# Kernel optimization log

Measured on AMD Instinct MI355X. Metric: run time of the kernel, lower is better.

The kernel has to match this reference:

```python
import jax, jax.numpy as jnp
import numpy as np

B, N, E, M = 16, 128, 127, 16
BN = B * N
BNE = B * N * E


def _ln(x, g, b):
    mu = x.mean(-1, keepdims=True)
    var = ((x - mu) ** 2).mean(-1, keepdims=True)
    return (x - mu) * jax.lax.rsqrt(var + 1e-5) * g + b


def _radial(feat, w1, b1, g1, be1, w2, b2, g2, be2, w3, b3, nf):
    # Linear -> LayerNorm -> ReLU -> Linear -> LayerNorm -> ReLU -> Linear
    h = jax.nn.relu(_ln(feat @ w1.T + b1, g1, be1))
    h = jax.nn.relu(_ln(h @ w2.T + b2, g2, be2))
    y = h @ w3.T + b3
    return y.reshape(-1, M, 1, M, 1, nf)  # [BN, out_ch, 1, in_ch, 1, num_freq]


def _kernel(R, basis, do):
    K = (R * basis).sum(-1)  # [BN, M, 2do+1, M, 2di+1]
    return K.reshape(K.shape[0], (2 * do + 1) * M, -1)


def setup_inputs() -> dict:
    key = jax.random.key(0)
    ks = jax.random.split(key, 16)
    d = {}
    d["r"] = jax.random.uniform(ks[0], (BNE, 1), jnp.float32)
    d["src0"] = jax.random.normal(ks[1], (BNE, M, 1), jnp.float32)
    d["src1"] = jax.random.normal(ks[2], (BNE, M, 3), jnp.float32)
    d["basis_00"] = jax.random.normal(ks[3], (BN, 1, 1, 1, 1, 1), jnp.float32)
    d["basis_01"] = jax.random.normal(ks[4], (BN, 1, 3, 1, 1, 1), jnp.float32)
    d["basis_10"] = jax.random.normal(ks[5], (BN, 1, 1, 1, 3, 1), jnp.float32)
    d["basis_11"] = jax.random.normal(ks[6], (BN, 1, 3, 1, 3, 3), jnp.float32)
    d["w1"] = jax.random.normal(ks[7], (4, 32, 1), jnp.float32) * 0.5
    d["b1"] = jnp.zeros((4, 32), jnp.float32)
    d["g1"] = jnp.ones((4, 32), jnp.float32)
    d["be1"] = jnp.zeros((4, 32), jnp.float32)
    d["w2"] = jax.random.normal(ks[8], (4, 32, 32), jnp.float32) * 0.18
    d["b2"] = jnp.zeros((4, 32), jnp.float32)
    d["g2"] = jnp.ones((4, 32), jnp.float32)
    d["be2"] = jnp.zeros((4, 32), jnp.float32)
    d["w3_00"] = jax.random.normal(ks[9], (1 * M * M, 32), jnp.float32) * 0.18
    d["b3_00"] = jnp.zeros((1 * M * M,), jnp.float32)
    d["w3_01"] = jax.random.normal(ks[10], (1 * M * M, 32), jnp.float32) * 0.18
    d["b3_01"] = jnp.zeros((1 * M * M,), jnp.float32)
    d["w3_10"] = jax.random.normal(ks[11], (1 * M * M, 32), jnp.float32) * 0.18
    d["b3_10"] = jnp.zeros((1 * M * M,), jnp.float32)
    d["w3_11"] = jax.random.normal(ks[12], (3 * M * M, 32), jnp.float32) * 0.18
    d["b3_11"] = jnp.zeros((3 * M * M,), jnp.float32)
    return d


def reference(r, src0, src1, basis_00, basis_01, basis_10, basis_11,
              w1, b1, g1, be1, w2, b2, g2, be2,
              w3_00, b3_00, w3_01, b3_01, w3_10, b3_10, w3_11, b3_11):
    # reduce per-edge tensors to the representative (first) edge of each node,
    # exactly as the original's view(B,N,E,...)[:, :, 0] does
    feat = r.reshape(B, N, E, -1)[:, :, 0, :].reshape(BN, -1)             # [BN, 1]
    s0 = src0.reshape(B, N, E, M * 1, 1)[:, :, 0].reshape(BN, M * 1, 1)   # [BN, 16, 1]
    s1 = src1.reshape(B, N, E, M * 3, 1)[:, :, 0].reshape(BN, M * 48 // M, 1)  # [BN, 48, 1]

    # per-(d_in, d_out) kernels; param index 0=(0,0) 1=(0,1) 2=(1,0) 3=(1,1)
    K00 = _kernel(_radial(feat, w1[0], b1[0], g1[0], be1[0], w2[0], b2[0], g2[0], be2[0], w3_00, b3_00, 1), basis_00, 0)
    K01 = _kernel(_radial(feat, w1[1], b1[1], g1[1], be1[1], w2[1], b2[1], g2[1], be2[1], w3_01, b3_01, 1), basis_01, 1)
    K10 = _kernel(_radial(feat, w1[2], b1[2], g1[2], be1[2], w2[2], b2[2], g2[2], be2[2], w3_10, b3_10, 1), basis_10, 0)
    K11 = _kernel(_radial(feat, w1[3], b1[3], g1[3], be1[3], w2[3], b2[3], g2[3], be2[3], w3_11, b3_11, 3), basis_11, 1)

    msg0 = K00 @ s0 + K10 @ s1  # [BN, 16, 1]  (degree-0 output)
    msg1 = K01 @ s0 + K11 @ s1  # [BN, 48, 1]  (degree-1 output)

    # broadcast per-node message to every edge of that node
    out0 = jnp.broadcast_to(msg0.reshape(B, N, 1, M, 1), (B, N, E, M, 1)).reshape(BNE, M, 1)
    out1 = jnp.broadcast_to(msg1.reshape(B, N, 1, M * 3, 1), (B, N, E, M * 3, 1)).reshape(BNE, M, 3)
    return out0, out1
```

## Files before the change

### kernel.cpp

```cpp
#include <hip/hip_runtime.h>

#define E_ 127
#define NB 8
#define OUT0_F4 1040384
#define O0_PER_NODE_F4 508
#define O1_PER_NODE_F4 1524

__device__ __forceinline__ float red32(float v) {
    v += __shfl_xor(v, 1, 32);
    v += __shfl_xor(v, 2, 32);
    v += __shfl_xor(v, 4, 32);
    v += __shfl_xor(v, 8, 32);
    v += __shfl_xor(v, 16, 32);
    return v;
}

__global__ __launch_bounds__(256) void msg_kernel(
    const float* __restrict__ r,   const float* __restrict__ src0, const float* __restrict__ src1,
    const float* __restrict__ b00, const float* __restrict__ b01,
    const float* __restrict__ b10, const float* __restrict__ b11,
    const float* __restrict__ w1,  const float* __restrict__ bb1,
    const float* __restrict__ g1,  const float* __restrict__ be1,
    const float* __restrict__ w2,  const float* __restrict__ bb2,
    const float* __restrict__ g2,  const float* __restrict__ be2,
    const float* __restrict__ w300, const float* __restrict__ b300,
    const float* __restrict__ w301, const float* __restrict__ b301,
    const float* __restrict__ w310, const float* __restrict__ b310,
    const float* __restrict__ w311, const float* __restrict__ b311,
    float* __restrict__ msg_out)
{
    __shared__ float s0s[NB][16];
    __shared__ float s1s[NB][48];
    __shared__ float t1s[NB][16];
    __shared__ float us[NB][3][16][3];
    __shared__ float b00s[NB];
    __shared__ float b01s[NB][3];
    __shared__ float b10s[NB][3];
    __shared__ float b11s[NB][27];
    __shared__ float feats[NB];
    __shared__ float h2s[4][NB][32];
    __shared__ float Rl[NB][1537];

    const int tid = threadIdx.x;
    const int n0 = blockIdx.x * NB;

    for (int idx = tid; idx < NB * 16; idx += 256) {
        int nn = idx >> 4, m = idx & 15;
        s0s[nn][m] = src0[(size_t)(n0 + nn) * E_ * 16 + m];
    }
    for (int idx = tid; idx < NB * 48; idx += 256) {
        int nn = idx / 48, j = idx % 48;
        s1s[nn][j] = src1[(size_t)(n0 + nn) * E_ * 48 + j];
    }
    if (tid < NB) {
        b00s[tid]  = b00[n0 + tid];
        feats[tid] = r[(size_t)(n0 + tid) * E_];
    }
    if (tid >= 32 && tid < 32 + NB * 3) {
        int q = tid - 32; int nn = q / 3, d = q % 3;
        b01s[nn][d] = b01[(size_t)(n0 + nn) * 3 + d];
    }
    if (tid >= 64 && tid < 64 + NB * 3) {
        int q = tid - 64; int nn = q / 3, c = q % 3;
        b10s[nn][c] = b10[(size_t)(n0 + nn) * 3 + c];
    }
    for (int idx = tid; idx < NB * 27; idx += 256) {
        int nn = idx / 27, q = idx % 27;
        b11s[nn][q] = b11[(size_t)(n0 + nn) * 27 + q];
    }
    __syncthreads();

    for (int idx = tid; idx < NB * 16; idx += 256) {
        int nn = idx >> 4, i = idx & 15;
        t1s[nn][i] = b10s[nn][0] * s1s[nn][i*3]
                   + b10s[nn][1] * s1s[nn][i*3+1]
                   + b10s[nn][2] * s1s[nn][i*3+2];
    }
    for (int idx = tid; idx < NB * 144; idx += 256) {
        int nn = idx / 144, q = idx % 144;
        int d = q / 48, q2 = q % 48, i = q2 / 3, f = q2 % 3;
        float a = 0.f;
        #pragma unroll
        for (int c = 0; c < 3; ++c) a += b11s[nn][d*9 + c*3 + f] * s1s[nn][i*3 + c];
        us[nn][d][i][f] = a;
    }

    {
        const int g = tid >> 5;
        const int j = tid & 31;
        #pragma unroll
        for (int p = 0; p < 4; ++p) {
            float h = feats[g] * w1[p*32 + j] + bb1[p*32 + j];
            float mu = red32(h) * (1.0f/32.0f);
            float dv = h - mu;
            float var = red32(dv*dv) * (1.0f/32.0f);
            float x = dv * rsqrtf(var + 1e-5f) * g1[p*32 + j] + be1[p*32 + j];
            float h1n = fmaxf(x, 0.0f);

            const float4* w2v = (const float4*)(w2 + p*1024 + j*32);
            float acc = bb2[p*32 + j];
            #pragma unroll
            for (int k4 = 0; k4 < 8; ++k4) {
                float4 w = w2v[k4];
                acc += __shfl(h1n, 4*k4 + 0, 32) * w.x;
                acc += __shfl(h1n, 4*k4 + 1, 32) * w.y;
                acc += __shfl(h1n, 4*k4 + 2, 32) * w.z;
                acc += __shfl(h1n, 4*k4 + 3, 32) * w.w;
            }
            mu = red32(acc) * (1.0f/32.0f);
            dv = acc - mu;
            var = red32(dv*dv) * (1.0f/32.0f);
            x = dv * rsqrtf(var + 1e-5f) * g2[p*32 + j] + be2[p*32 + j];
            h2s[p][g][j] = fmaxf(x, 0.0f);
        }
    }
    __syncthreads();

    for (int rr = 0; rr < 6; ++rr) {
        int idx = tid + rr * 256;
        const float* W; const float* Bv; int p, row;
        if (idx < 256)      { p = 0; row = idx;       W = w300; Bv = b300; }
        else if (idx < 512) { p = 1; row = idx - 256; W = w301; Bv = b301; }
        else if (idx < 768) { p = 2; row = idx - 512; W = w310; Bv = b310; }
        else                { p = 3; row = idx - 768; W = w311; Bv = b311; }
        const float4* wv = (const float4*)(W + row * 32);
        float4 a0 = wv[0], a1 = wv[1], a2 = wv[2], a3 = wv[3];
        float4 a4 = wv[4], a5 = wv[5], a6 = wv[6], a7 = wv[7];
        float bb = Bv[row];
        #pragma unroll
        for (int nn = 0; nn < NB; ++nn) {
            const float* h = h2s[p][nn];
            float acc = bb;
            acc += a0.x*h[0]  + a0.y*h[1]  + a0.z*h[2]  + a0.w*h[3];
            acc += a1.x*h[4]  + a1.y*h[5]  + a1.z*h[6]  + a1.w*h[7];
            acc += a2.x*h[8]  + a2.y*h[9]  + a2.z*h[10] + a2.w*h[11];
            acc += a3.x*h[12] + a3.y*h[13] + a3.z*h[14] + a3.w*h[15];
            acc += a4.x*h[16] + a4.y*h[17] + a4.z*h[18] + a4.w*h[19];
            acc += a5.x*h[20] + a5.y*h[21] + a5.z*h[22] + a5.w*h[23];
            acc += a6.x*h[24] + a6.y*h[25] + a6.z*h[26] + a6.w*h[27];
            acc += a7.x*h[28] + a7.y*h[29] + a7.z*h[30] + a7.w*h[31];
            Rl[nn][idx] = acc;
        }
    }
    __syncthreads();

    for (int pair = tid; pair < 512; pair += 256) {
        if (pair < 128) {
            int o = pair >> 3, nn = pair & 7;
            const float* Rn = Rl[nn];
            float acc0 = 0.f, acc2 = 0.f;
            #pragma unroll
            for (int i = 0; i < 16; ++i) {
                acc0 += Rn[o*16 + i]       * s0s[nn][i];
                acc2 += Rn[512 + o*16 + i] * t1s[nn][i];
            }
            msg_out[(size_t)(n0 + nn) * 64 + o] = b00s[nn] * acc0 + acc2;
        } else {
            int q = pair - 128;
            int od = q >> 3, nn = q & 7;
            int o = od / 3, d = od % 3;
            const float* Rn = Rl[nn];
            float acc1 = 0.f, acc3 = 0.f;
            #pragma unroll
            for (int i = 0; i < 16; ++i) {
                acc1 += Rn[256 + o*16 + i] * s0s[nn][i];
                #pragma unroll
                for (int f = 0; f < 3; ++f)
                    acc3 += Rn[768 + (o*16 + i)*3 + f] * us[nn][d][i][f];
            }
            msg_out[(size_t)(n0 + nn) * 64 + 16 + od] = b01s[nn][d] * acc1 + acc3;
        }
    }
}

__global__ __launch_bounds__(256) void bcast_kernel(const float* __restrict__ msg,
                                                    float* __restrict__ out)
{
    __shared__ float4 m0v[4];
    __shared__ float4 m1v[12];
    const int n = blockIdx.x;
    const int tid = threadIdx.x;
    if (tid < 16) {
        float4 v = ((const float4*)(msg + (size_t)n * 64))[tid];
        if (tid < 4) m0v[tid] = v; else m1v[tid - 4] = v;
    }
    __syncthreads();

    float4* o0 = (float4*)out + (size_t)n * O0_PER_NODE_F4;
    for (int k = tid; k < O0_PER_NODE_F4; k += 256)
        o0[k] = m0v[k & 3];

    float4* o1 = (float4*)out + OUT0_F4 + (size_t)n * O1_PER_NODE_F4;
    for (int k = tid; k < O1_PER_NODE_F4; k += 256)
        o1[k] = m1v[k % 12];
}

extern "C" void kernel_launch(void* const* d_in, const int* in_sizes, int n_in,
                              void* d_out, int out_size, void* d_ws, size_t ws_size,
                              hipStream_t stream)
{
    const float* r    = (const float*)d_in[0];
    const float* src0 = (const float*)d_in[1];
    const float* src1 = (const float*)d_in[2];
    const float* b00  = (const float*)d_in[3];
    const float* b01  = (const float*)d_in[4];
    const float* b10  = (const float*)d_in[5];
    const float* b11  = (const float*)d_in[6];
    const float* w1   = (const float*)d_in[7];
    const float* bb1  = (const float*)d_in[8];
    const float* g1   = (const float*)d_in[9];
    const float* be1  = (const float*)d_in[10];
    const float* w2   = (const float*)d_in[11];
    const float* bb2  = (const float*)d_in[12];
    const float* g2   = (const float*)d_in[13];
    const float* be2  = (const float*)d_in[14];
    const float* w300 = (const float*)d_in[15];
    const float* b300 = (const float*)d_in[16];
    const float* w301 = (const float*)d_in[17];
    const float* b301 = (const float*)d_in[18];
    const float* w310 = (const float*)d_in[19];
    const float* b310 = (const float*)d_in[20];
    const float* w311 = (const float*)d_in[21];
    const float* b311 = (const float*)d_in[22];

    float* msg = (float*)d_ws;

    msg_kernel<<<256, 256, 0, stream>>>(r, src0, src1, b00, b01, b10, b11,
        w1, bb1, g1, be1, w2, bb2, g2, be2,
        w300, b300, w301, b301, w310, b310, w311, b311, msg);

    bcast_kernel<<<2048, 256, 0, stream>>>(msg, (float*)d_out);
}
```

Measured before the change: 172.5 us.

## Fuse message computation and edge broadcast into one kernel with smaller node batches

Merges the per-node message kernel and the broadcast kernel into a single kernel, so messages stay in shared memory and go straight to the output without a workspace round trip or a second launch. The node batch per block is halved so the grid doubles to 512 blocks. Thread-to-work mappings for loads, the radial MLP and the contraction are remapped to fit 4 nodes per block. In exchange, the bandwidth-bound broadcast now runs on only 512 blocks that must first finish the MLP compute, which may reduce store parallelism.

```diff
diff --git a/kernel.cpp b/kernel.cpp
--- a/kernel.cpp
+++ b/kernel.cpp
@@ -1,7 +1,7 @@
 #include <hip/hip_runtime.h>
 
 #define E_ 127
-#define NB 8
+#define NB 4
 #define OUT0_F4 1040384
 #define O0_PER_NODE_F4 508
 #define O1_PER_NODE_F4 1524
@@ -15,7 +15,7 @@
     return v;
 }
 
-__global__ __launch_bounds__(256) void msg_kernel(
+__global__ __launch_bounds__(256) void fused_kernel(
     const float* __restrict__ r,   const float* __restrict__ src0, const float* __restrict__ src1,
     const float* __restrict__ b00, const float* __restrict__ b01,
     const float* __restrict__ b10, const float* __restrict__ b11,
@@ -27,7 +27,7 @@
     const float* __restrict__ w301, const float* __restrict__ b301,
     const float* __restrict__ w310, const float* __restrict__ b310,
     const float* __restrict__ w311, const float* __restrict__ b311,
-    float* __restrict__ msg_out)
+    float* __restrict__ out)
 {
     __shared__ float s0s[NB][16];
     __shared__ float s1s[NB][48];
@@ -40,45 +40,46 @@
     __shared__ float feats[NB];
     __shared__ float h2s[4][NB][32];
     __shared__ float Rl[NB][1537];
+    __shared__ float msgs[NB][64];
 
     const int tid = threadIdx.x;
     const int n0 = blockIdx.x * NB;
 
-    for (int idx = tid; idx < NB * 16; idx += 256) {
-        int nn = idx >> 4, m = idx & 15;
+    if (tid < NB * 16) {
+        int nn = tid >> 4, m = tid & 15;
         s0s[nn][m] = src0[(size_t)(n0 + nn) * E_ * 16 + m];
     }
-    for (int idx = tid; idx < NB * 48; idx += 256) {
-        int nn = idx / 48, j = idx % 48;
+    if (tid >= 64 && tid < 64 + NB * 48) {
+        int q = tid - 64; int nn = q / 48, j = q % 48;
         s1s[nn][j] = src1[(size_t)(n0 + nn) * E_ * 48 + j];
     }
     if (tid < NB) {
         b00s[tid]  = b00[n0 + tid];
         feats[tid] = r[(size_t)(n0 + tid) * E_];
     }
-    if (tid >= 32 && tid < 32 + NB * 3) {
-        int q = tid - 32; int nn = q / 3, d = q % 3;
+    if (tid >= 8 && tid < 8 + NB * 3) {
+        int q = tid - 8; int nn = q / 3, d = q % 3;
         b01s[nn][d] = b01[(size_t)(n0 + nn) * 3 + d];
     }
-    if (tid >= 64 && tid < 64 + NB * 3) {
-        int q = tid - 64; int nn = q / 3, c = q % 3;
+    if (tid >= 24 && tid < 24 + NB * 3) {
+        int q = tid - 24; int nn = q / 3, c = q % 3;
         b10s[nn][c] = b10[(size_t)(n0 + nn) * 3 + c];
     }
-    for (int idx = tid; idx < NB * 27; idx += 256) {
-        int nn = idx / 27, q = idx % 27;
-        b11s[nn][q] = b11[(size_t)(n0 + nn) * 27 + q];
-    }
-    __syncthreads();
-
-    for (int idx = tid; idx < NB * 16; idx += 256) {
-        int nn = idx >> 4, i = idx & 15;
+    if (tid >= 40 && tid < 40 + NB * 27) {
+        int q = tid - 40; int nn = q / 27, qq = q % 27;
+        b11s[nn][qq] = b11[(size_t)(n0 + nn) * 27 + qq];
+    }
+    __syncthreads();
+
+    if (tid < NB * 16) {
+        int nn = tid >> 4, i = tid & 15;
         t1s[nn][i] = b10s[nn][0] * s1s[nn][i*3]
                    + b10s[nn][1] * s1s[nn][i*3+1]
                    + b10s[nn][2] * s1s[nn][i*3+2];
     }
     for (int idx = tid; idx < NB * 144; idx += 256) {
-        int nn = idx / 144, q = idx % 144;
-        int d = q / 48, q2 = q % 48, i = q2 / 3, f = q2 % 3;
+        int nn = idx / 144, qq = idx % 144;
+        int d = qq / 48, q2 = qq % 48, i = q2 / 3, f = q2 % 3;
         float a = 0.f;
         #pragma unroll
         for (int c = 0; c < 3; ++c) a += b11s[nn][d*9 + c*3 + f] * s1s[nn][i*3 + c];
@@ -88,9 +89,12 @@
     {
         const int g = tid >> 5;
         const int j = tid & 31;
+        const int nn = g >> 1;
+        const int p0 = (g & 1) * 2;
         #pragma unroll
-        for (int p = 0; p < 4; ++p) {
-            float h = feats[g] * w1[p*32 + j] + bb1[p*32 + j];
+        for (int pi = 0; pi < 2; ++pi) {
+            const int p = p0 + pi;
+            float h = feats[nn] * w1[p*32 + j] + bb1[p*32 + j];
             float mu = red32(h) * (1.0f/32.0f);
             float dv = h - mu;
             float var = red32(dv*dv) * (1.0f/32.0f);
@@ -111,7 +115,7 @@
             dv = acc - mu;
             var = red32(dv*dv) * (1.0f/32.0f);
             x = dv * rsqrtf(var + 1e-5f) * g2[p*32 + j] + be2[p*32 + j];
-            h2s[p][g][j] = fmaxf(x, 0.0f);
+            h2s[p][nn][j] = fmaxf(x, 0.0f);
         }
     }
     __syncthreads();
@@ -144,9 +148,10 @@
     }
     __syncthreads();
 
-    for (int pair = tid; pair < 512; pair += 256) {
-        if (pair < 128) {
-            int o = pair >> 3, nn = pair & 7;
+    {
+        const int pair = tid;
+        if (pair < 64) {
+            int o = pair >> 2, nn = pair & 3;
             const float* Rn = Rl[nn];
             float acc0 = 0.f, acc2 = 0.f;
             #pragma unroll
@@ -154,10 +159,10 @@
                 acc0 += Rn[o*16 + i]       * s0s[nn][i];
                 acc2 += Rn[512 + o*16 + i] * t1s[nn][i];
             }
-            msg_out[(size_t)(n0 + nn) * 64 + o] = b00s[nn] * acc0 + acc2;
+            msgs[nn][o] = b00s[nn] * acc0 + acc2;
         } else {
-            int q = pair - 128;
-            int od = q >> 3, nn = q & 7;
+            int q = pair - 64;
+            int od = q >> 2, nn = q & 3;
             int o = od / 3, d = od % 3;
             const float* Rn = Rl[nn];
             float acc1 = 0.f, acc3 = 0.f;
@@ -168,31 +173,22 @@
                 for (int f = 0; f < 3; ++f)
                     acc3 += Rn[768 + (o*16 + i)*3 + f] * us[nn][d][i][f];
             }
-            msg_out[(size_t)(n0 + nn) * 64 + 16 + od] = b01s[nn][d] * acc1 + acc3;
+            msgs[nn][16 + od] = b01s[nn][d] * acc1 + acc3;
         }
     }
-}
-
-__global__ __launch_bounds__(256) void bcast_kernel(const float* __restrict__ msg,
-                                                    float* __restrict__ out)
-{
-    __shared__ float4 m0v[4];
-    __shared__ float4 m1v[12];
-    const int n = blockIdx.x;
-    const int tid = threadIdx.x;
-    if (tid < 16) {
-        float4 v = ((const float4*)(msg + (size_t)n * 64))[tid];
-        if (tid < 4) m0v[tid] = v; else m1v[tid - 4] = v;
-    }
-    __syncthreads();
-
-    float4* o0 = (float4*)out + (size_t)n * O0_PER_NODE_F4;
-    for (int k = tid; k < O0_PER_NODE_F4; k += 256)
-        o0[k] = m0v[k & 3];
-
-    float4* o1 = (float4*)out + OUT0_F4 + (size_t)n * O1_PER_NODE_F4;
-    for (int k = tid; k < O1_PER_NODE_F4; k += 256)
-        o1[k] = m1v[k % 12];
+    __syncthreads();
+
+    const float4* mv = (const float4*)&msgs[0][0];
+    #pragma unroll
+    for (int nn = 0; nn < NB; ++nn) {
+        const int node = n0 + nn;
+        float4* o0 = (float4*)out + (size_t)node * O0_PER_NODE_F4;
+        for (int k = tid; k < O0_PER_NODE_F4; k += 256)
+            o0[k] = mv[nn*16 + (k & 3)];
+        float4* o1 = (float4*)out + OUT0_F4 + (size_t)node * O1_PER_NODE_F4;
+        for (int k = tid; k < O1_PER_NODE_F4; k += 256)
+            o1[k] = mv[nn*16 + 4 + (k % 12)];
+    }
 }
 
 extern "C" void kernel_launch(void* const* d_in, const int* in_sizes, int n_in,
@@ -223,11 +219,7 @@
     const float* w311 = (const float*)d_in[21];
     const float* b311 = (const float*)d_in[22];
 
-    float* msg = (float*)d_ws;
-
-    msg_kernel<<<256, 256, 0, stream>>>(r, src0, src1, b00, b01, b10, b11,
+    fused_kernel<<<512, 256, 0, stream>>>(r, src0, src1, b00, b01, b10, b11,
         w1, bb1, g1, be1, w2, bb2, g2, be2,
-        w300, b300, w301, b301, w310, b310, w311, b311, msg);
-
-    bcast_kernel<<<2048, 256, 0, stream>>>(msg, (float*)d_out);
+        w300, b300, w301, b301, w310, b310, w311, b311, (float*)d_out);
 }
```

Result: faster. 165.7 us, median of 2 (-4.0%).
